# Optimization experiments

Hardware: AMD Instinct MI355X
Metric: run time of the kernel (lower is better)

Reference implementation:

```python
import jax, jax.numpy as jnp
import numpy as np
from jax import lax

N_LAYERS = 10
N_BLOCKS = 3
N_STACK = N_LAYERS * N_BLOCKS  # 30
WIDTH = 512
SKIP_W = 256
CH = 1
QUANT = 256
BOTTLENECK = 16
KSIZE = 3
SCALE = 2 ** (N_LAYERS - 1)  # 512, nearest upsample factor
B, T = 1, 16384
T_EMB = T // SCALE  # 32


def causal_conv(x, w, b, dilation):
    # x: [B,Cin,T], w: [Cout,Cin,K] -> causal dilated conv, output [B,Cout,T]
    k = w.shape[-1]
    pad = (k - 1) * dilation
    y = lax.conv_general_dilated(x, w, window_strides=(1,), padding=[(pad, 0)],
                                 rhs_dilation=(dilation,),
                                 dimension_numbers=('NCH', 'OIH', 'NCH'))
    return y + b[None, :, None]


def conv1x1(x, w, b):
    # x: [B,Cin,T], w: [Cout,Cin]
    return jnp.einsum('oc,bct->bot', w, x) + b[None, :, None]


def setup_inputs() -> dict:
    key = jax.random.key(0)
    ks = jax.random.split(key, 24)
    s = 0.05
    inp = {
        'x': jax.random.normal(ks[0], (B, CH, T), jnp.float32),
        'embedding': jax.random.normal(ks[1], (B, BOTTLENECK, T_EMB), jnp.float32),
        'w_init': jax.random.normal(ks[2], (WIDTH, CH, KSIZE), jnp.float32) * s,
        'b_init': jnp.zeros((WIDTH,), jnp.float32),
        'w_iskip': jax.random.normal(ks[3], (SKIP_W, WIDTH), jnp.float32) * s,
        'b_iskip': jnp.zeros((SKIP_W,), jnp.float32),
        'w_dil': jax.random.normal(ks[4], (N_STACK, 2 * WIDTH, WIDTH, KSIZE), jnp.float32) * s,
        'b_dil': jnp.zeros((N_STACK, 2 * WIDTH), jnp.float32),
        'w_cond': jax.random.normal(ks[5], (N_STACK, 2 * WIDTH, BOTTLENECK), jnp.float32) * s,
        'b_cond': jnp.zeros((N_STACK, 2 * WIDTH), jnp.float32),
        'w_res': jax.random.normal(ks[6], (N_STACK, WIDTH, WIDTH), jnp.float32) * s,
        'b_res': jnp.zeros((N_STACK, WIDTH), jnp.float32),
        'w_skip': jax.random.normal(ks[7], (N_STACK, SKIP_W, WIDTH), jnp.float32) * s,
        'b_skip': jnp.zeros((N_STACK, SKIP_W), jnp.float32),
        'w_fskip': jax.random.normal(ks[8], (SKIP_W, SKIP_W), jnp.float32) * s,
        'b_fskip': jnp.zeros((SKIP_W,), jnp.float32),
        'w_fcond': jax.random.normal(ks[9], (SKIP_W, BOTTLENECK), jnp.float32) * s,
        'b_fcond': jnp.zeros((SKIP_W,), jnp.float32),
        'w_quant': jax.random.normal(ks[10], (QUANT, SKIP_W), jnp.float32) * s,
        'b_quant': jnp.zeros((QUANT,), jnp.float32),
    }
    return inp


def reference(x, embedding, w_init, b_init, w_iskip, b_iskip, w_dil, b_dil,
              w_cond, b_cond, w_res, b_res, w_skip, b_skip,
              w_fskip, b_fskip, w_fcond, b_fcond, w_quant, b_quant):
    # initial causal conv (kernel 3, dilation 1) + initial skip 1x1
    h = causal_conv(x, w_init, b_init, 1)            # [B,WIDTH,T]
    skip = conv1x1(h, w_iskip, b_iskip)              # [B,SKIP_W,T]
    for i in range(N_STACK):
        dilation = 2 ** (i % N_LAYERS)
        cond = conv1x1(embedding, w_cond[i], b_cond[i])      # [B,2W,T_EMB]
        cond_up = jnp.repeat(cond, SCALE, axis=-1)           # nearest upsample -> [B,2W,T]
        dilated = causal_conv(h, w_dil[i], b_dil[i], dilation) + cond_up
        filters = jax.nn.sigmoid(dilated[:, :WIDTH, :])
        gates = jnp.tanh(dilated[:, WIDTH:, :])
        pre = filters * gates
        h = h + conv1x1(pre, w_res[i], b_res[i])
        skip = skip + conv1x1(pre, w_skip[i], b_skip[i])
    skip = conv1x1(jax.nn.relu(skip), w_fskip, b_fskip)
    fcond = jnp.repeat(conv1x1(embedding, w_fcond, b_fcond), SCALE, axis=-1)
    skip = skip + fcond
    return conv1x1(jax.nn.relu(skip), w_quant, b_quant)     # [B,QUANT,T]
```

## Files before the change

### kernel.cpp

```cpp
#include <hip/hip_runtime.h>


typedef _Float16 f16x8 __attribute__((ext_vector_type(8)));
typedef float f32x4 __attribute__((ext_vector_type(4)));

#define NSTACK 30
#define TLEN   16384

typedef __attribute__((address_space(1))) const unsigned int glob_u32;
typedef __attribute__((address_space(3))) unsigned int lds_u32;

__device__ __forceinline__ void gll16(const unsigned short* g, unsigned short* l) {
  __builtin_amdgcn_global_load_lds((glob_u32*)g, (lds_u32*)l, 16, 0, 0);
}

__device__ __forceinline__ unsigned short f2h(float x) {
  union { _Float16 h; unsigned short u; } c;
  c.h = (_Float16)x;
  return c.u;
}
__device__ __forceinline__ unsigned pack2(float a, float b) {
  return (unsigned)f2h(a) | ((unsigned)f2h(b) << 16);
}
__device__ __forceinline__ f16x8 ldh(const unsigned short* p) {
  return *(const f16x8*)p;
}
__device__ __forceinline__ float sigmoidf_(float x){ return 1.0f/(1.0f+__expf(-x)); }
__device__ __forceinline__ float tanhf_(float x){ return 1.0f - 2.0f/(__expf(2.0f*x)+1.0f); }
#define MFMA16(a,b,c) __builtin_amdgcn_mfma_f32_16x16x32_f16((a),(b),(c),0,0,0)


__global__ void cast_f16_kernel(const float* __restrict__ src,
                                unsigned short* __restrict__ dst, int n4) {
  int g = blockIdx.x*256 + threadIdx.x;
  if (g >= n4) return;
  f32x4 v = *(const f32x4*)(src + 4*(size_t)g);
  unsigned int* d = (unsigned int*)(dst + 4*(size_t)g);
  d[0] = pack2(v[0], v[1]);
  d[1] = pack2(v[2], v[3]);
}

__global__ void transpose_wdil_kernel(const float* __restrict__ src,
                                      unsigned short* __restrict__ dst) {
  int g = blockIdx.x*256 + threadIdx.x;
  if (g >= NSTACK*1024*512) return;
  int c = g & 511;
  int m = (g >> 9) & 1023;
  int i = g >> 19;
  const float* s = src + (size_t)g*3;
  #pragma unroll
  for (int tap=0; tap<3; ++tap)
    dst[(((size_t)i*3+tap)*1024 + m)*512 + c] = f2h(s[tap]);
}

__global__ void cond_kernel(const float* __restrict__ emb,
                            const float* __restrict__ w_cond, const float* __restrict__ b_cond,
                            const float* __restrict__ b_dil,
                            const float* __restrict__ w_fcond, const float* __restrict__ b_fcond,
                            float* __restrict__ cond_all, float* __restrict__ fcond_all) {
  int g = blockIdx.x*256 + threadIdx.x;
  if (g < NSTACK*1024) {
    float acc[32];
    float base = b_cond[g] + b_dil[g];
    #pragma unroll
    for (int e=0;e<32;++e) acc[e] = base;
    #pragma unroll
    for (int c=0;c<16;++c) {
      float wv = w_cond[(size_t)g*16 + c];
      #pragma unroll
      for (int e=0;e<32;++e) acc[e] += wv * emb[c*32+e];
    }
    #pragma unroll
    for (int e=0;e<32;++e) cond_all[(size_t)g*32+e] = acc[e];
  } else if (g < NSTACK*1024 + 256) {
    int m = g - NSTACK*1024;
    float acc[32];
    float base = b_fcond[m];
    #pragma unroll
    for (int e=0;e<32;++e) acc[e] = base;
    #pragma unroll
    for (int c=0;c<16;++c) {
      float wv = w_fcond[(size_t)m*16 + c];
      #pragma unroll
      for (int e=0;e<32;++e) acc[e] += wv * emb[c*32+e];
    }
    #pragma unroll
    for (int e=0;e<32;++e) fcond_all[(size_t)m*32+e] = acc[e];
  }
}

__global__ void h0_kernel(const float* __restrict__ x, const float* __restrict__ w_init,
                          const float* __restrict__ b_init,
                          float* __restrict__ h_f32, unsigned short* __restrict__ h_h16) {
  int g = blockIdx.x*256 + threadIdx.x;
  int t = g >> 7;
  int c = (g & 127) << 2;
  float xm2 = (t>=2)? x[t-2] : 0.f;
  float xm1 = (t>=1)? x[t-1] : 0.f;
  float x0  = x[t];
  f32x4 hv;
  #pragma unroll
  for (int r=0;r<4;++r) {
    int cc = c + r;
    hv[r] = w_init[cc*3+0]*xm2 + w_init[cc*3+1]*xm1 + w_init[cc*3+2]*x0 + b_init[cc];
  }
  *(f32x4*)&h_f32[(size_t)t*512 + c] = hv;
  unsigned int* hb = (unsigned int*)&h_h16[(size_t)t*512 + c];
  hb[0] = pack2(hv[0],hv[1]); hb[1] = pack2(hv[2],hv[3]);
}

__global__ __launch_bounds__(512) void skip_init_kernel(
    const unsigned short* __restrict__ h_h16, const unsigned short* __restrict__ Wiskip,
    const float* __restrict__ b_iskip, float* __restrict__ skip_f32) {
  int tid=threadIdx.x, w=tid>>6, l=tid&63, lr=l&15, lc=l>>4;
  int tb = blockIdx.x<<6;
  f32x4 acc[2][4];
  #pragma unroll
  for (int mf=0;mf<2;++mf)
    #pragma unroll
    for (int nf=0;nf<4;++nf) acc[mf][nf] = {0.f,0.f,0.f,0.f};
  for (int kc=0;kc<512;kc+=32) {
    f16x8 b[4];
    #pragma unroll
    for (int nf=0;nf<4;++nf)
      b[nf] = ldh(&h_h16[(size_t)(tb+16*nf+lr)*512 + kc + lc*8]);
    #pragma unroll
    for (int mf=0;mf<2;++mf) {
      f16x8 a = ldh(&Wiskip[(size_t)(w*32+16*mf+lr)*512 + kc + lc*8]);
      #pragma unroll
      for (int nf=0;nf<4;++nf)
        acc[mf][nf] = MFMA16(a, b[nf], acc[mf][nf]);
    }
  }
  #pragma unroll
  for (int mf=0;mf<2;++mf)
    #pragma unroll
    for (int nf=0;nf<4;++nf) {
      int s0 = w*32+16*mf+4*lc;
      int t  = tb+16*nf+lr;
      f32x4 v;
      #pragma unroll
      for (int r=0;r<4;++r) v[r] = acc[mf][nf][r] + b_iskip[s0+r];
      *(f32x4*)&skip_f32[(size_t)t*256+s0] = v;
    }
}

__global__ __launch_bounds__(256, 3) void dil_kernel(
    const unsigned short* __restrict__ h_in,
    unsigned short* __restrict__ pre,
    const unsigned short* __restrict__ A_dil,
    const float* __restrict__ cond,
    const unsigned short* __restrict__ zerobuf,
    int dilation) {
  __shared__ unsigned short Ab[2][128][32];
  __shared__ unsigned short Bb[2][128][32];
  const int tid = threadIdx.x;
  const int w = tid >> 6, l = tid & 63;
  const int lr = l & 15, lc = l >> 4;
  const int nt = blockIdx.x & 127, mt = blockIdx.x >> 7;
  const int tb = nt << 7;
  const int e  = tb >> 9;
  const int wr = w >> 1, wc = w & 1;

  const int srowA0 = (w<<5) + (l>>2);
  const int schunk = (l & 3) << 3;

  f32x4 fa[2][4], ga[2][4];
  #pragma unroll
  for (int mf=0;mf<2;++mf)
    #pragma unroll
    for (int nf=0;nf<4;++nf) { fa[mf][nf] = {0.f,0.f,0.f,0.f}; ga[mf][nf] = {0.f,0.f,0.f,0.f}; }

  auto stage = [&](int buf, int s){
    const int tap = s >> 4;
    const int kc  = (s & 15) << 5;
    const int shift = (2 - tap) * dilation;
    const unsigned short* Abase = A_dil + (size_t)tap * (1024*512) + kc + schunk;
    #pragma unroll
    for (int j=0;j<2;++j){
      const int r = srowA0 + (j<<4);
      const int m = mt*64 + r + ((r>>6)*448);
      gll16(Abase + (size_t)m*512, &Ab[buf][(w<<5)+(j<<4)][0]);
      const int t = tb + r - shift;
      const unsigned short* srcB = (t >= 0) ? (h_in + (size_t)t*512 + kc + schunk)
                                            : (zerobuf + schunk);
      gll16(srcB, &Bb[buf][(w<<5)+(j<<4)][0]);
    }
  };

  stage(0, 0);
  for (int s=0; s<48; ++s) {
    const int cur = s & 1;
    __syncthreads();
    if (s+1 < 48) stage(cur^1, s+1);
    f16x8 af[2], ag[2], bf[4];
    #pragma unroll
    for (int mf=0;mf<2;++mf){
      const int row = (wr<<5) + (mf<<4) + lr;
      af[mf] = ldh(&Ab[cur][row][lc<<3]);
      ag[mf] = ldh(&Ab[cur][64+row][lc<<3]);
    }
    #pragma unroll
    for (int nf=0;nf<4;++nf)
      bf[nf] = ldh(&Bb[cur][(wc<<6)+(nf<<4)+lr][lc<<3]);
    #pragma unroll
    for (int mf=0;mf<2;++mf)
      #pragma unroll
      for (int nf=0;nf<4;++nf){
        fa[mf][nf] = MFMA16(af[mf], bf[nf], fa[mf][nf]);
        ga[mf][nf] = MFMA16(ag[mf], bf[nf], ga[mf][nf]);
      }
  }

  #pragma unroll
  for (int mf=0;mf<2;++mf)
    #pragma unroll
    for (int nf=0;nf<4;++nf){
      const int m0 = mt*64 + (wr<<5) + (mf<<4) + (lc<<2);
      const int t  = tb + (wc<<6) + (nf<<4) + lr;
      float pv[4];
      #pragma unroll
      for (int r=0;r<4;++r){
        float f = fa[mf][nf][r] + cond[(size_t)(m0+r)*32 + e];
        float g = ga[mf][nf][r] + cond[(size_t)(m0+r+512)*32 + e];
        pv[r] = sigmoidf_(f) * tanhf_(g);
      }
      unsigned int* pp = (unsigned int*)&pre[(size_t)t*512 + m0];
      pp[0] = pack2(pv[0], pv[1]);
      pp[1] = pack2(pv[2], pv[3]);
    }
}

__global__ __launch_bounds__(256, 3) void ressk_kernel(
    const unsigned short* __restrict__ pre,
    unsigned short* __restrict__ h_out,
    float* __restrict__ h_f32,
    float* __restrict__ skip_f32,
    const unsigned short* __restrict__ Wres,
    const unsigned short* __restrict__ Wskip,
    const float* __restrict__ b_res,
    const float* __restrict__ b_skip) {
  __shared__ unsigned short Ab[2][64][32];
  __shared__ unsigned short Bb[2][128][32];
  const int tid = threadIdx.x;
  const int w = tid >> 6, l = tid & 63;
  const int lr = l & 15, lc = l >> 4;
  const int nt = blockIdx.x & 127, mt = blockIdx.x >> 7;
  const int tb = nt << 7;
  const int wr = w >> 1, wc = w & 1;
  const bool isres = (mt < 8);
  const unsigned short* W = isres ? Wres : Wskip;
  const int mrow0 = (isres ? mt : (mt-8)) * 64;

  const int srowA = (w<<4) + (l>>2);
  const int srowB0 = (w<<5) + (l>>2);
  const int schunk = (l & 3) << 3;

  f32x4 acc[2][4];
  #pragma unroll
  for (int mf=0;mf<2;++mf)
    #pragma unroll
    for (int nf=0;nf<4;++nf) acc[mf][nf] = {0.f,0.f,0.f,0.f};

  auto stage = [&](int buf, int s){
    const int kc = s << 5;
    gll16(W + (size_t)(mrow0 + srowA)*512 + kc + schunk, &Ab[buf][(w<<4)][0]);
    #pragma unroll
    for (int j=0;j<2;++j){
      const int t = tb + srowB0 + (j<<4);
      gll16(pre + (size_t)t*512 + kc + schunk, &Bb[buf][(w<<5)+(j<<4)][0]);
    }
  };

  stage(0, 0);
  for (int s=0; s<16; ++s) {
    const int cur = s & 1;
    __syncthreads();
    if (s+1 < 16) stage(cur^1, s+1);
    f16x8 a[2], bf[4];
    #pragma unroll
    for (int mf=0;mf<2;++mf)
      a[mf] = ldh(&Ab[cur][(wr<<5)+(mf<<4)+lr][lc<<3]);
    #pragma unroll
    for (int nf=0;nf<4;++nf)
      bf[nf] = ldh(&Bb[cur][(wc<<6)+(nf<<4)+lr][lc<<3]);
    #pragma unroll
    for (int mf=0;mf<2;++mf)
      #pragma unroll
      for (int nf=0;nf<4;++nf)
        acc[mf][nf] = MFMA16(a[mf], bf[nf], acc[mf][nf]);
  }

  if (isres) {
    #pragma unroll
    for (int mf=0;mf<2;++mf)
      #pragma unroll
      for (int nf=0;nf<4;++nf){
        const int m0 = mrow0 + (wr<<5) + (mf<<4) + (lc<<2);
        const int t  = tb + (wc<<6) + (nf<<4) + lr;
        f32x4* hp = (f32x4*)&h_f32[(size_t)t*512 + m0];
        f32x4 hv = *hp;
        #pragma unroll
        for (int r=0;r<4;++r) hv[r] += acc[mf][nf][r] + b_res[m0+r];
        *hp = hv;
        unsigned int* hb = (unsigned int*)&h_out[(size_t)t*512 + m0];
        hb[0] = pack2(hv[0],hv[1]); hb[1] = pack2(hv[2],hv[3]);
      }
  } else {
    #pragma unroll
    for (int mf=0;mf<2;++mf)
      #pragma unroll
      for (int nf=0;nf<4;++nf){
        const int s0 = mrow0 + (wr<<5) + (mf<<4) + (lc<<2);
        const int t  = tb + (wc<<6) + (nf<<4) + lr;
        f32x4* sp = (f32x4*)&skip_f32[(size_t)t*256 + s0];
        f32x4 sv = *sp;
        #pragma unroll
        for (int r=0;r<4;++r) sv[r] += acc[mf][nf][r] + b_skip[s0+r];
        *sp = sv;
      }
  }
}

__global__ __launch_bounds__(512) void final_kernel(
    const float* __restrict__ skip_f32, const unsigned short* __restrict__ Wfs,
    const float* __restrict__ b_fskip, const float* __restrict__ fcond,
    const unsigned short* __restrict__ Wq, const float* __restrict__ b_quant,
    float* __restrict__ out) {
  __shared__ unsigned short S1[64][264];
  __shared__ unsigned short S2[64][264];
  int tid=threadIdx.x, w=tid>>6, l=tid&63, lr=l&15, lc=l>>4;
  int tb = blockIdx.x<<6, e = tb>>9;

  for (int j = tid; j < 64*64; j += 512) {
    int r  = j >> 6;
    int c4 = (j & 63) << 2;
    f32x4 v = *(const f32x4*)&skip_f32[(size_t)(tb+r)*256 + c4];
    #pragma unroll
    for (int q=0;q<4;++q) v[q] = fmaxf(v[q], 0.f);
    unsigned int* sp = (unsigned int*)&S1[r][c4];
    sp[0] = pack2(v[0],v[1]); sp[1] = pack2(v[2],v[3]);
  }
  __syncthreads();

  f32x4 acc[2][4];
  #pragma unroll
  for (int mf=0;mf<2;++mf)
    #pragma unroll
    for (int nf=0;nf<4;++nf) acc[mf][nf] = {0.f,0.f,0.f,0.f};
  for (int kc=0;kc<256;kc+=32) {
    f16x8 b[4];
    #pragma unroll
    for (int nf=0;nf<4;++nf) b[nf] = ldh(&S1[16*nf+lr][kc + lc*8]);
    #pragma unroll
    for (int mf=0;mf<2;++mf) {
      f16x8 a = ldh(&Wfs[(size_t)(w*32+16*mf+lr)*256 + kc + lc*8]);
      #pragma unroll
      for (int nf=0;nf<4;++nf)
        acc[mf][nf] = MFMA16(a, b[nf], acc[mf][nf]);
    }
  }
  #pragma unroll
  for (int mf=0;mf<2;++mf)
    #pragma unroll
    for (int nf=0;nf<4;++nf) {
      int m0 = w*32+16*mf+4*lc;
      int n  = 16*nf+lr;
      float pv[4];
      #pragma unroll
      for (int r=0;r<4;++r) {
        float v = acc[mf][nf][r] + b_fskip[m0+r] + fcond[(size_t)(m0+r)*32 + e];
        pv[r] = fmaxf(v, 0.f);
      }
      unsigned int* pp = (unsigned int*)&S2[n][m0];
      pp[0] = pack2(pv[0],pv[1]); pp[1] = pack2(pv[2],pv[3]);
    }
  __syncthreads();

  f32x4 acc2[2][4];
  #pragma unroll
  for (int mf=0;mf<2;++mf)
    #pragma unroll
    for (int nf=0;nf<4;++nf) acc2[mf][nf] = {0.f,0.f,0.f,0.f};
  for (int kc=0;kc<256;kc+=32) {
    f16x8 b[4];
    #pragma unroll
    for (int nf=0;nf<4;++nf) b[nf] = ldh(&S2[16*nf+lr][kc + lc*8]);
    #pragma unroll
    for (int mf=0;mf<2;++mf) {
      f16x8 a = ldh(&Wq[(size_t)(w*32+16*mf+lr)*256 + kc + lc*8]);
      #pragma unroll
      for (int nf=0;nf<4;++nf)
        acc2[mf][nf] = MFMA16(a, b[nf], acc2[mf][nf]);
    }
  }
  #pragma unroll
  for (int mf=0;mf<2;++mf)
    #pragma unroll
    for (int nf=0;nf<4;++nf) {
      int q0 = w*32+16*mf+4*lc;
      int t  = tb + 16*nf + lr;
      #pragma unroll
      for (int r=0;r<4;++r)
        out[(size_t)(q0+r)*TLEN + t] = acc2[mf][nf][r] + b_quant[q0+r];
    }
}


extern "C" void kernel_launch(void* const* d_in, const int* in_sizes, int n_in,
                              void* d_out, int out_size, void* d_ws, size_t ws_size,
                              hipStream_t stream) {
  const float* x       = (const float*)d_in[0];
  const float* emb     = (const float*)d_in[1];
  const float* w_init  = (const float*)d_in[2];
  const float* b_init  = (const float*)d_in[3];
  const float* w_iskip = (const float*)d_in[4];
  const float* b_iskip = (const float*)d_in[5];
  const float* w_dil   = (const float*)d_in[6];
  const float* b_dil   = (const float*)d_in[7];
  const float* w_cond  = (const float*)d_in[8];
  const float* b_cond  = (const float*)d_in[9];
  const float* w_res   = (const float*)d_in[10];
  const float* b_res   = (const float*)d_in[11];
  const float* w_skip  = (const float*)d_in[12];
  const float* b_skip  = (const float*)d_in[13];
  const float* w_fskip = (const float*)d_in[14];
  const float* b_fskip = (const float*)d_in[15];
  const float* w_fcond = (const float*)d_in[16];
  const float* b_fcond = (const float*)d_in[17];
  const float* w_quant = (const float*)d_in[18];
  const float* b_quant = (const float*)d_in[19];
  float* out = (float*)d_out;

  char* ws = (char*)d_ws;
  size_t off = 0;
  auto carve = [&](size_t bytes) -> void* {
    void* p = ws + off;
    off += (bytes + 255) & ~(size_t)255;
    return p;
  };
  unsigned short* A_dil     = (unsigned short*)carve((size_t)NSTACK*3*1024*512*2);
  unsigned short* Wres_h    = (unsigned short*)carve((size_t)NSTACK*512*512*2);
  unsigned short* Wskip_h   = (unsigned short*)carve((size_t)NSTACK*256*512*2);
  unsigned short* Wiskip_h  = (unsigned short*)carve((size_t)256*512*2);
  unsigned short* Wfskip_h  = (unsigned short*)carve((size_t)256*256*2);
  unsigned short* Wquant_h  = (unsigned short*)carve((size_t)256*256*2);
  float*          h_f32     = (float*)carve((size_t)TLEN*512*4);
  unsigned short* h_h16     = (unsigned short*)carve((size_t)2*TLEN*512*2);
  unsigned short* pre_h16   = (unsigned short*)carve((size_t)TLEN*512*2);
  float*          skip_f32  = (float*)carve((size_t)TLEN*256*4);
  float*          cond_all  = (float*)carve((size_t)NSTACK*1024*32*4);
  float*          fcond_all = (float*)carve((size_t)256*32*4);
  unsigned short* zerobuf   = (unsigned short*)carve((size_t)512*2);
  if (off > ws_size) return;

  hipMemsetAsync(zerobuf, 0, 512*2, stream);

  cast_f16_kernel<<<(NSTACK*512*512/4 + 255)/256, 256, 0, stream>>>(w_res,   Wres_h,   NSTACK*512*512/4);
  cast_f16_kernel<<<(NSTACK*256*512/4 + 255)/256, 256, 0, stream>>>(w_skip,  Wskip_h,  NSTACK*256*512/4);
  cast_f16_kernel<<<(256*512/4 + 255)/256,        256, 0, stream>>>(w_iskip, Wiskip_h, 256*512/4);
  cast_f16_kernel<<<(256*256/4 + 255)/256,        256, 0, stream>>>(w_fskip, Wfskip_h, 256*256/4);
  cast_f16_kernel<<<(256*256/4 + 255)/256,        256, 0, stream>>>(w_quant, Wquant_h, 256*256/4);
  transpose_wdil_kernel<<<(NSTACK*1024*512 + 255)/256, 256, 0, stream>>>(w_dil, A_dil);
  cond_kernel<<<(NSTACK*1024 + 256 + 255)/256, 256, 0, stream>>>(
      emb, w_cond, b_cond, b_dil, w_fcond, b_fcond, cond_all, fcond_all);

  h0_kernel<<<TLEN*128/256, 256, 0, stream>>>(x, w_init, b_init, h_f32, h_h16);
  skip_init_kernel<<<TLEN/64, 512, 0, stream>>>(h_h16, Wiskip_h, b_iskip, skip_f32);

  const size_t HB = (size_t)TLEN*512;
  for (int i = 0; i < NSTACK; ++i) {
    int d = 1 << (i % 10);
    dil_kernel<<<1024, 256, 0, stream>>>(
        h_h16 + (size_t)(i & 1)*HB,
        pre_h16,
        A_dil + (size_t)i*3*1024*512,
        cond_all + (size_t)i*1024*32,
        zerobuf,
        d);
    ressk_kernel<<<1536, 256, 0, stream>>>(
        pre_h16,
        h_h16 + (size_t)((i + 1) & 1)*HB,
        h_f32, skip_f32,
        Wres_h + (size_t)i*512*512,
        Wskip_h + (size_t)i*256*512,
        b_res + (size_t)i*512,
        b_skip + (size_t)i*256);
  }

  final_kernel<<<TLEN/64, 512, 0, stream>>>(
      skip_f32, Wfskip_h, b_fskip, fcond_all, Wquant_h, b_quant, out);
}
```

Before: 3.489 ms.

## Triple-buffer LDS staging with vmcnt waits and XCD-aware block remap

Switches dil_kernel and ressk_kernel from double- to triple-buffered LDS staging. Loads for step s+2 are issued while step s computes, with partial s_waitcnt vmcnt replacing the full __syncthreads drain. It also remaps block IDs so consecutive time tiles land on the same XCD, aiming for better L2 reuse of the activations, and raises ressk_kernel's launch_bounds occupancy hint to 4. The cost is more LDS per block, which may lower occupancy, plus reliance on hand-counted vmcnt values being correct.

```diff
diff --git a/kernel.cpp b/kernel.cpp
--- a/kernel.cpp
+++ b/kernel.cpp
@@ -152,12 +152,16 @@
     const float* __restrict__ cond,
     const unsigned short* __restrict__ zerobuf,
     int dilation) {
-  __shared__ unsigned short Ab[2][128][32];
-  __shared__ unsigned short Bb[2][128][32];
+  __shared__ unsigned short Ab[3][128][32];
+  __shared__ unsigned short Bb[3][128][32];
   const int tid = threadIdx.x;
   const int w = tid >> 6, l = tid & 63;
   const int lr = l & 15, lc = l >> 4;
-  const int nt = blockIdx.x & 127, mt = blockIdx.x >> 7;
+  const int bid = blockIdx.x;
+  const int xcd = bid & 7;
+  const int idx = bid >> 3;
+  const int nt  = xcd*16 + (idx & 15);
+  const int mt  = idx >> 4;
   const int tb = nt << 7;
   const int e  = tb >> 9;
   const int wr = w >> 1, wc = w & 1;
@@ -189,10 +193,13 @@
   };
 
   stage(0, 0);
+  stage(1, 1);
   for (int s=0; s<48; ++s) {
-    const int cur = s & 1;
-    __syncthreads();
-    if (s+1 < 48) stage(cur^1, s+1);
+    const int cur = s % 3;
+    if (s + 1 < 48) { asm volatile("s_waitcnt vmcnt(4)" ::: "memory"); }
+    else            { asm volatile("s_waitcnt vmcnt(0)" ::: "memory"); }
+    __builtin_amdgcn_s_barrier();
+    if (s + 2 < 48) stage((s+2) % 3, s+2);
     f16x8 af[2], ag[2], bf[4];
     #pragma unroll
     for (int mf=0;mf<2;++mf){
@@ -231,7 +238,7 @@
     }
 }
 
-__global__ __launch_bounds__(256, 3) void ressk_kernel(
+__global__ __launch_bounds__(256, 4) void ressk_kernel(
     const unsigned short* __restrict__ pre,
     unsigned short* __restrict__ h_out,
     float* __restrict__ h_f32,
@@ -240,12 +247,16 @@
     const unsigned short* __restrict__ Wskip,
     const float* __restrict__ b_res,
     const float* __restrict__ b_skip) {
-  __shared__ unsigned short Ab[2][64][32];
-  __shared__ unsigned short Bb[2][128][32];
+  __shared__ unsigned short Ab[3][64][32];
+  __shared__ unsigned short Bb[3][128][32];
   const int tid = threadIdx.x;
   const int w = tid >> 6, l = tid & 63;
   const int lr = l & 15, lc = l >> 4;
-  const int nt = blockIdx.x & 127, mt = blockIdx.x >> 7;
+  const int bid = blockIdx.x;
+  const int xcd = bid & 7;
+  const int idx = bid >> 3;
+  const int nt  = xcd*16 + (idx & 15);
+  const int mt  = idx >> 4;
   const int tb = nt << 7;
   const int wr = w >> 1, wc = w & 1;
   const bool isres = (mt < 8);
@@ -273,10 +284,13 @@
   };
 
   stage(0, 0);
+  stage(1, 1);
   for (int s=0; s<16; ++s) {
-    const int cur = s & 1;
-    __syncthreads();
-    if (s+1 < 16) stage(cur^1, s+1);
+    const int cur = s % 3;
+    if (s + 1 < 16) { asm volatile("s_waitcnt vmcnt(3)" ::: "memory"); }
+    else            { asm volatile("s_waitcnt vmcnt(0)" ::: "memory"); }
+    __builtin_amdgcn_s_barrier();
+    if (s + 2 < 16) stage((s+2) % 3, s+2);
     f16x8 a[2], bf[4];
     #pragma unroll
     for (int mf=0;mf<2;++mf)
```

New measurement: 3.837 ms. 1.1x slower.

## Enlarge GEMM tiles to 256x256 with 8 waves and split-phase prefetch

Applied to the files above, without the earlier changes.

Both the dilated-conv and the res/skip GEMM kernels move to 512-thread blocks with 256x256 output tiles and 64-wide K steps. The loads for the next K tile are spread across four compute phases using explicit s_barrier/vmcnt waits and s_setprio around the MFMA bursts. This raises arithmetic intensity and cuts redundant global traffic and barriers per FLOP. The cost is much higher register and LDS use per block and far fewer blocks: 256 and 192 on a GPU with 256 CUs, so ressk underfills the device and each launch has a longer tail.

```diff
diff --git a/kernel.cpp b/kernel.cpp
--- a/kernel.cpp
+++ b/kernel.cpp
@@ -28,6 +28,8 @@
 __device__ __forceinline__ float sigmoidf_(float x){ return 1.0f/(1.0f+__expf(-x)); }
 __device__ __forceinline__ float tanhf_(float x){ return 1.0f - 2.0f/(__expf(2.0f*x)+1.0f); }
 #define MFMA16(a,b,c) __builtin_amdgcn_mfma_f32_16x16x32_f16((a),(b),(c),0,0,0)
+#define BAR_FENCE() asm volatile("s_barrier" ::: "memory")
+#define VMCNT0()    asm volatile("s_waitcnt vmcnt(0)" ::: "memory")
 
 
 __global__ void cast_f16_kernel(const float* __restrict__ src,
@@ -145,84 +147,104 @@
     }
 }
 
-__global__ __launch_bounds__(256, 3) void dil_kernel(
+__global__ __launch_bounds__(512, 2) void dil_kernel(
     const unsigned short* __restrict__ h_in,
     unsigned short* __restrict__ pre,
     const unsigned short* __restrict__ A_dil,
     const float* __restrict__ cond,
     const unsigned short* __restrict__ zerobuf,
     int dilation) {
-  __shared__ unsigned short Ab[2][128][32];
-  __shared__ unsigned short Bb[2][128][32];
+  __shared__ unsigned short SA[2][16384];
+  __shared__ unsigned short SB[2][16384];
   const int tid = threadIdx.x;
   const int w = tid >> 6, l = tid & 63;
   const int lr = l & 15, lc = l >> 4;
-  const int nt = blockIdx.x & 127, mt = blockIdx.x >> 7;
-  const int tb = nt << 7;
-  const int e  = tb >> 9;
-  const int wr = w >> 1, wc = w & 1;
-
-  const int srowA0 = (w<<5) + (l>>2);
-  const int schunk = (l & 3) << 3;
-
-  f32x4 fa[2][4], ga[2][4];
-  #pragma unroll
-  for (int mf=0;mf<2;++mf)
-    #pragma unroll
-    for (int nf=0;nf<4;++nf) { fa[mf][nf] = {0.f,0.f,0.f,0.f}; ga[mf][nf] = {0.f,0.f,0.f,0.f}; }
-
-  auto stage = [&](int buf, int s){
-    const int tap = s >> 4;
-    const int kc  = (s & 15) << 5;
-    const int shift = (2 - tap) * dilation;
-    const unsigned short* Abase = A_dil + (size_t)tap * (1024*512) + kc + schunk;
-    #pragma unroll
-    for (int j=0;j<2;++j){
-      const int r = srowA0 + (j<<4);
-      const int m = mt*64 + r + ((r>>6)*448);
-      gll16(Abase + (size_t)m*512, &Ab[buf][(w<<5)+(j<<4)][0]);
-      const int t = tb + r - shift;
-      const unsigned short* srcB = (t >= 0) ? (h_in + (size_t)t*512 + kc + schunk)
-                                            : (zerobuf + schunk);
-      gll16(srcB, &Bb[buf][(w<<5)+(j<<4)][0]);
+  const int wr = w >> 2, wc = w & 3;
+  const int mt = blockIdx.x >> 6, nt = blockIdx.x & 63;
+  const int tb = nt << 8;
+  const int fm0 = mt << 7;
+  const int e = tb >> 9;
+
+  f32x4 facc[4][4], gacc[4][4];
+  #pragma unroll
+  for (int mf=0;mf<4;++mf)
+    #pragma unroll
+    for (int nf=0;nf<4;++nf){ facc[mf][nf] = {0.f,0.f,0.f,0.f}; gacc[mf][nf] = {0.f,0.f,0.f,0.f}; }
+
+  const int srow16 = l & 15;
+  const int skch0  = l >> 4;
+
+  auto stageHalf = [&](int buf, int ktp, int hf){
+    const int tap = ktp >> 3;
+    const int kin = (ktp & 7) << 6;
+    unsigned short* base = (hf < 2) ? &SA[buf][hf*8192] : &SB[buf][(hf-2)*8192];
+    #pragma unroll
+    for (int jj=0; jj<2; ++jj){
+      unsigned short* dst = base + w*1024 + jj*512;
+      const int kch = skch0 + jj*4;
+      if (hf < 2){
+        const int r = hf*128 + w*16 + srow16;
+        const int m = fm0 + ((r>>7)&1)*64 + (r&63) + (((r>>6)&1)<<9);
+        gll16(A_dil + (size_t)tap*524288 + (size_t)m*512 + kin + kch*8, dst);
+      } else {
+        const int shift = (2 - tap) * dilation;
+        const int t = tb + (hf-2)*128 + w*16 + srow16 - shift;
+        const unsigned short* src = (t >= 0) ? (h_in + (size_t)t*512 + kin + kch*8)
+                                             : (zerobuf + kch*8);
+        gll16(src, dst);
+      }
     }
   };
 
-  stage(0, 0);
-  for (int s=0; s<48; ++s) {
-    const int cur = s & 1;
-    __syncthreads();
-    if (s+1 < 48) stage(cur^1, s+1);
-    f16x8 af[2], ag[2], bf[4];
-    #pragma unroll
-    for (int mf=0;mf<2;++mf){
-      const int row = (wr<<5) + (mf<<4) + lr;
-      af[mf] = ldh(&Ab[cur][row][lc<<3]);
-      ag[mf] = ldh(&Ab[cur][64+row][lc<<3]);
-    }
-    #pragma unroll
-    for (int nf=0;nf<4;++nf)
-      bf[nf] = ldh(&Bb[cur][(wc<<6)+(nf<<4)+lr][lc<<3]);
-    #pragma unroll
-    for (int mf=0;mf<2;++mf)
-      #pragma unroll
-      for (int nf=0;nf<4;++nf){
-        fa[mf][nf] = MFMA16(af[mf], bf[nf], fa[mf][nf]);
-        ga[mf][nf] = MFMA16(ag[mf], bf[nf], ga[mf][nf]);
-      }
-  }
-
-  #pragma unroll
-  for (int mf=0;mf<2;++mf)
+  #pragma unroll
+  for (int hf=0; hf<4; ++hf) stageHalf(0, 0, hf);
+
+  for (int kt=0; kt<24; ++kt){
+    const int cur = kt & 1;
+    const unsigned short* Abase = &SA[cur][wr*8192];
+    const unsigned short* Bbase = &SB[cur][(wc>>1)*8192];
+    #pragma unroll
+    for (int p=0; p<4; ++p){
+      if (p == 0){ VMCNT0(); BAR_FENCE(); }
+      const int mg = p & 1, kh = p >> 1;
+      f16x8 af[4], bf[4];
+      #pragma unroll
+      for (int mf=0; mf<4; ++mf)
+        af[mf] = ldh(Abase + (mg*4+mf)*1024 + (kh*4+lc)*128 + lr*8);
+      #pragma unroll
+      for (int nf=0; nf<4; ++nf)
+        bf[nf] = ldh(Bbase + ((wc&1)*4+nf)*1024 + (kh*4+lc)*128 + lr*8);
+      if (kt + 1 < 24) stageHalf(cur^1, kt+1, p);
+      BAR_FENCE();
+      __builtin_amdgcn_s_setprio(1);
+      if (mg == 0){
+        #pragma unroll
+        for (int mf=0;mf<4;++mf)
+          #pragma unroll
+          for (int nf=0;nf<4;++nf)
+            facc[mf][nf] = MFMA16(af[mf], bf[nf], facc[mf][nf]);
+      } else {
+        #pragma unroll
+        for (int mf=0;mf<4;++mf)
+          #pragma unroll
+          for (int nf=0;nf<4;++nf)
+            gacc[mf][nf] = MFMA16(af[mf], bf[nf], gacc[mf][nf]);
+      }
+      __builtin_amdgcn_s_setprio(0);
+    }
+  }
+
+  #pragma unroll
+  for (int mf=0;mf<4;++mf)
     #pragma unroll
     for (int nf=0;nf<4;++nf){
-      const int m0 = mt*64 + (wr<<5) + (mf<<4) + (lc<<2);
-      const int t  = tb + (wc<<6) + (nf<<4) + lr;
+      const int m0 = fm0 + wr*64 + mf*16 + lc*4;
+      const int t  = tb + wc*64 + nf*16 + lr;
       float pv[4];
       #pragma unroll
       for (int r=0;r<4;++r){
-        float f = fa[mf][nf][r] + cond[(size_t)(m0+r)*32 + e];
-        float g = ga[mf][nf][r] + cond[(size_t)(m0+r+512)*32 + e];
+        float f = facc[mf][nf][r] + cond[(size_t)(m0+r)*32 + e];
+        float g = gacc[mf][nf][r] + cond[(size_t)(m0+r+512)*32 + e];
         pv[r] = sigmoidf_(f) * tanhf_(g);
       }
       unsigned int* pp = (unsigned int*)&pre[(size_t)t*512 + m0];
@@ -231,7 +253,7 @@
     }
 }
 
-__global__ __launch_bounds__(256, 3) void ressk_kernel(
+__global__ __launch_bounds__(512, 2) void ressk_kernel(
     const unsigned short* __restrict__ pre,
     unsigned short* __restrict__ h_out,
     float* __restrict__ h_f32,
@@ -240,64 +262,88 @@
     const unsigned short* __restrict__ Wskip,
     const float* __restrict__ b_res,
     const float* __restrict__ b_skip) {
-  __shared__ unsigned short Ab[2][64][32];
-  __shared__ unsigned short Bb[2][128][32];
+  __shared__ unsigned short SA[2][16384];
+  __shared__ unsigned short SB[2][16384];
   const int tid = threadIdx.x;
   const int w = tid >> 6, l = tid & 63;
   const int lr = l & 15, lc = l >> 4;
-  const int nt = blockIdx.x & 127, mt = blockIdx.x >> 7;
-  const int tb = nt << 7;
-  const int wr = w >> 1, wc = w & 1;
-  const bool isres = (mt < 8);
-  const unsigned short* W = isres ? Wres : Wskip;
-  const int mrow0 = (isres ? mt : (mt-8)) * 64;
-
-  const int srowA = (w<<4) + (l>>2);
-  const int srowB0 = (w<<5) + (l>>2);
-  const int schunk = (l & 3) << 3;
-
-  f32x4 acc[2][4];
-  #pragma unroll
-  for (int mf=0;mf<2;++mf)
+  const int wr = w >> 2, wc = w & 3;
+  const int mt = blockIdx.x >> 6, nt = blockIdx.x & 63;
+  const int tb = nt << 8;
+  const bool isres = (mt < 2);
+  const unsigned short* Wbase = isres ? (Wres + (size_t)mt*256*512) : Wskip;
+
+  f32x4 acc[8][4];
+  #pragma unroll
+  for (int mf=0;mf<8;++mf)
     #pragma unroll
     for (int nf=0;nf<4;++nf) acc[mf][nf] = {0.f,0.f,0.f,0.f};
 
-  auto stage = [&](int buf, int s){
-    const int kc = s << 5;
-    gll16(W + (size_t)(mrow0 + srowA)*512 + kc + schunk, &Ab[buf][(w<<4)][0]);
-    #pragma unroll
-    for (int j=0;j<2;++j){
-      const int t = tb + srowB0 + (j<<4);
-      gll16(pre + (size_t)t*512 + kc + schunk, &Bb[buf][(w<<5)+(j<<4)][0]);
+  const int srow16 = l & 15;
+  const int skch0  = l >> 4;
+
+  auto stageHalf = [&](int buf, int ktp, int hf){
+    const int kin = ktp << 6;
+    unsigned short* base = (hf < 2) ? &SA[buf][hf*8192] : &SB[buf][(hf-2)*8192];
+    #pragma unroll
+    for (int jj=0; jj<2; ++jj){
+      unsigned short* dst = base + w*1024 + jj*512;
+      const int kch = skch0 + jj*4;
+      if (hf < 2){
+        const int r = hf*128 + w*16 + srow16;
+        gll16(Wbase + (size_t)r*512 + kin + kch*8, dst);
+      } else {
+        const int t = tb + (hf-2)*128 + w*16 + srow16;
+        gll16(pre + (size_t)t*512 + kin + kch*8, dst);
+      }
     }
   };
 
-  stage(0, 0);
-  for (int s=0; s<16; ++s) {
-    const int cur = s & 1;
-    __syncthreads();
-    if (s+1 < 16) stage(cur^1, s+1);
-    f16x8 a[2], bf[4];
-    #pragma unroll
-    for (int mf=0;mf<2;++mf)
-      a[mf] = ldh(&Ab[cur][(wr<<5)+(mf<<4)+lr][lc<<3]);
-    #pragma unroll
-    for (int nf=0;nf<4;++nf)
-      bf[nf] = ldh(&Bb[cur][(wc<<6)+(nf<<4)+lr][lc<<3]);
-    #pragma unroll
-    for (int mf=0;mf<2;++mf)
-      #pragma unroll
-      for (int nf=0;nf<4;++nf)
-        acc[mf][nf] = MFMA16(a[mf], bf[nf], acc[mf][nf]);
+  #pragma unroll
+  for (int hf=0; hf<4; ++hf) stageHalf(0, 0, hf);
+
+  for (int kt=0; kt<8; ++kt){
+    const int cur = kt & 1;
+    const unsigned short* Abase = &SA[cur][wr*8192];
+    const unsigned short* Bbase = &SB[cur][(wc>>1)*8192];
+    #pragma unroll
+    for (int p=0; p<4; ++p){
+      if (p == 0){ VMCNT0(); BAR_FENCE(); }
+      const int mg = p & 1, kh = p >> 1;
+      f16x8 af[4], bf[4];
+      #pragma unroll
+      for (int mf=0; mf<4; ++mf)
+        af[mf] = ldh(Abase + (mg*4+mf)*1024 + (kh*4+lc)*128 + lr*8);
+      #pragma unroll
+      for (int nf=0; nf<4; ++nf)
+        bf[nf] = ldh(Bbase + ((wc&1)*4+nf)*1024 + (kh*4+lc)*128 + lr*8);
+      if (kt + 1 < 8) stageHalf(cur^1, kt+1, p);
+      BAR_FENCE();
+      __builtin_amdgcn_s_setprio(1);
+      if (mg == 0){
+        #pragma unroll
+        for (int mf=0;mf<4;++mf)
+          #pragma unroll
+          for (int nf=0;nf<4;++nf)
+            acc[mf][nf] = MFMA16(af[mf], bf[nf], acc[mf][nf]);
+      } else {
+        #pragma unroll
+        for (int mf=0;mf<4;++mf)
+          #pragma unroll
+          for (int nf=0;nf<4;++nf)
+            acc[4+mf][nf] = MFMA16(af[mf], bf[nf], acc[4+mf][nf]);
+      }
+      __builtin_amdgcn_s_setprio(0);
+    }
   }
 
   if (isres) {
     #pragma unroll
-    for (int mf=0;mf<2;++mf)
+    for (int mf=0;mf<8;++mf)
       #pragma unroll
       for (int nf=0;nf<4;++nf){
-        const int m0 = mrow0 + (wr<<5) + (mf<<4) + (lc<<2);
-        const int t  = tb + (wc<<6) + (nf<<4) + lr;
+        const int m0 = mt*256 + wr*128 + mf*16 + lc*4;
+        const int t  = tb + wc*64 + nf*16 + lr;
         f32x4* hp = (f32x4*)&h_f32[(size_t)t*512 + m0];
         f32x4 hv = *hp;
         #pragma unroll
@@ -308,11 +354,11 @@
       }
   } else {
     #pragma unroll
-    for (int mf=0;mf<2;++mf)
+    for (int mf=0;mf<8;++mf)
       #pragma unroll
       for (int nf=0;nf<4;++nf){
-        const int s0 = mrow0 + (wr<<5) + (mf<<4) + (lc<<2);
-        const int t  = tb + (wc<<6) + (nf<<4) + lr;
+        const int s0 = wr*128 + mf*16 + lc*4;
+        const int t  = tb + wc*64 + nf*16 + lr;
         f32x4* sp = (f32x4*)&skip_f32[(size_t)t*256 + s0];
         f32x4 sv = *sp;
         #pragma unroll
@@ -471,14 +517,14 @@
   const size_t HB = (size_t)TLEN*512;
   for (int i = 0; i < NSTACK; ++i) {
     int d = 1 << (i % 10);
-    dil_kernel<<<1024, 256, 0, stream>>>(
+    dil_kernel<<<256, 512, 0, stream>>>(
         h_h16 + (size_t)(i & 1)*HB,
         pre_h16,
         A_dil + (size_t)i*3*1024*512,
         cond_all + (size_t)i*1024*32,
         zerobuf,
         d);
-    ressk_kernel<<<1536, 256, 0, stream>>>(
+    ressk_kernel<<<192, 512, 0, stream>>>(
         pre_h16,
         h_h16 + (size_t)((i + 1) & 1)*HB,
         h_f32, skip_f32,
```

New measurement: 3.627 ms. +4.0%, slower.
